# Performance work log

Measured on AMD Instinct MI355X. Metric: run time of the kernel, lower is better.

## Reference

```python
import jax, jax.numpy as jnp
import numpy as np

B, L, QD, H, D = 2, 2048, 1024, 16, 64  # batch, seq, q_dim, heads, head_dim
INNER = H * D


def rms_norm(x, scale):
    # matches torch RMSNorm: mean over last dim in fp32, eps=1e-6, learned scale
    rrms = jax.lax.rsqrt(jnp.mean(x.astype(jnp.float32) ** 2, axis=-1, keepdims=True) + 1e-6)
    return (x * rrms).astype(x.dtype) * scale


def apply_rope(xq, xk, pe):
    # pe: [1,1,L,D//2,2,2] rotation-matrix pairs (FLUX-style)
    def rot(x):
        xs = x.reshape(*x.shape[:-1], D // 2, 1, 2)  # B H L D/2 1 2
        out = pe[..., 0] * xs[..., 0] + pe[..., 1] * xs[..., 1]  # B H L D/2 2
        return out.reshape(x.shape).astype(x.dtype)
    return rot(xq), rot(xk)


def setup_inputs() -> dict:
    key = jax.random.key(0)
    ks = jax.random.split(key, 6)
    s = 0.02
    return {
        "x": jax.random.normal(ks[0], (B, L, QD), jnp.float32),
        "pe": jax.random.normal(ks[1], (1, 1, L, D // 2, 2, 2), jnp.float32),
        "Wq": jax.random.normal(ks[2], (INNER, QD), jnp.float32) * s,
        "Wkv": jax.random.normal(ks[3], (2 * INNER, QD), jnp.float32) * s,
        "Wproj": jax.random.normal(ks[4], (QD, INNER), jnp.float32) * s,
        "bproj": jnp.zeros((QD,), jnp.float32),
        "q_scale": jnp.ones((D,), jnp.float32),
        "k_scale": jnp.ones((D,), jnp.float32),
    }


def reference(x, pe, Wq, Wkv, Wproj, bproj, q_scale, k_scale):
    # q/kv projections (self-attention: context = x)
    q = jnp.einsum('blc,ec->ble', x, Wq).reshape(B, L, H, D).transpose(0, 2, 1, 3)  # B H L D
    kv = jnp.einsum('blc,ec->ble', x, Wkv).reshape(B, L, 2, H, D)  # layout (K H D)
    k = kv[:, :, 0].transpose(0, 2, 1, 3)  # B H L D
    v = kv[:, :, 1].transpose(0, 2, 1, 3)  # B H L D
    # per-head QK RMSNorm
    q = rms_norm(q, q_scale)
    k = rms_norm(k, k_scale)
    # RoPE then scaled dot-product attention
    q, k = apply_rope(q, k, pe)
    scores = jnp.einsum('bhqd,bhkd->bhqk', q, k) / np.float32(np.sqrt(D))
    attn = jax.nn.softmax(scores, axis=-1)
    o = jnp.einsum('bhqk,bhkd->bhqd', attn, v)
    o = o.transpose(0, 2, 1, 3).reshape(B, L, INNER)  # B L (H D)
    return o @ Wproj.T + bproj
```

## Files before the change

kernel.cpp:

```cpp
#include <hip/hip_runtime.h>
#include <hip/hip_bf16.h>
#include <stdint.h>

#define BB 2
#define LL 2048
#define QDIM 1024
#define NH 16
#define HD 64

using bf16x8 = __attribute__((ext_vector_type(8))) __bf16;
using bf16x2 = __attribute__((ext_vector_type(2))) __bf16;
using f32x4  = __attribute__((ext_vector_type(4))) float;
using u16x8  = __attribute__((ext_vector_type(8))) unsigned short;
using u32x2  = __attribute__((ext_vector_type(2))) uint32_t;

__device__ __forceinline__ unsigned short f2bf(float f) {
  return __builtin_bit_cast(unsigned short, (__bf16)f);
}
__device__ __forceinline__ float bf2f(unsigned short h) {
  uint32_t u = ((uint32_t)h) << 16;
  return __builtin_bit_cast(float, u);
}
__device__ __forceinline__ uint32_t pkbf2(float a, float b) {
  bf16x2 v = { (__bf16)a, (__bf16)b };
  return __builtin_bit_cast(uint32_t, v);
}

__device__ __forceinline__ void gload_lds16(const void* g, void* l) {
  __builtin_amdgcn_global_load_lds((__attribute__((address_space(1))) void*)g,
                                   (__attribute__((address_space(3))) void*)l,
                                   16, 0, 0);
}

__global__ __launch_bounds__(256) void k_cast_bf16(const float* __restrict__ in,
                                                   unsigned short* __restrict__ out, int n) {
  int i = (blockIdx.x * 256 + threadIdx.x) * 8;
  if (i >= n) return;
  float4 a = *reinterpret_cast<const float4*>(in + i);
  float4 b = *reinterpret_cast<const float4*>(in + i + 4);
  u16x8 o;
  o[0] = f2bf(a.x); o[1] = f2bf(a.y); o[2] = f2bf(a.z); o[3] = f2bf(a.w);
  o[4] = f2bf(b.x); o[5] = f2bf(b.y); o[6] = f2bf(b.z); o[7] = f2bf(b.w);
  *reinterpret_cast<u16x8*>(out + i) = o;
}

__global__ __launch_bounds__(256) void k_gemm_qkv(const unsigned short* __restrict__ A,
                                                  const unsigned short* __restrict__ Bw,
                                                  unsigned short* __restrict__ qk,
                                                  unsigned short* __restrict__ vT) {
  __shared__ unsigned short As[2][128 * 32];
  __shared__ unsigned short Bs[2][128 * 32];
  const int t = threadIdx.x;
  const int lane = t & 63, w = t >> 6;
  const int wm = w >> 1, wn = w & 1;
  const int g = lane >> 4, r16 = lane & 15;
  const size_t am0 = (size_t)blockIdx.x * 128;
  const size_t bn0 = (size_t)blockIdx.y * 128;
  const int K = 1024;

  f32x4 acc[4][4] = {};

  const int o0 = t * 16, row0 = o0 >> 6, cb0 = o0 & 63;
  const int o1 = 4096 + t * 16, row1 = o1 >> 6, cb1 = o1 & 63;

  gload_lds16(A  + (am0 + row0) * K + (cb0 >> 1), (char*)&As[0][0] + o0);
  gload_lds16(A  + (am0 + row1) * K + (cb1 >> 1), (char*)&As[0][0] + o1);
  gload_lds16(Bw + (bn0 + row0) * K + (cb0 >> 1), (char*)&Bs[0][0] + o0);
  gload_lds16(Bw + (bn0 + row1) * K + (cb1 >> 1), (char*)&Bs[0][0] + o1);
  __syncthreads();

  for (int kb = 0; kb < K; kb += 32) {
    const int cur = (kb >> 5) & 1;
    if (kb + 32 < K) {
      const int nxt = cur ^ 1;
      gload_lds16(A  + (am0 + row0) * K + kb + 32 + (cb0 >> 1), (char*)&As[nxt][0] + o0);
      gload_lds16(A  + (am0 + row1) * K + kb + 32 + (cb1 >> 1), (char*)&As[nxt][0] + o1);
      gload_lds16(Bw + (bn0 + row0) * K + kb + 32 + (cb0 >> 1), (char*)&Bs[nxt][0] + o0);
      gload_lds16(Bw + (bn0 + row1) * K + kb + 32 + (cb1 >> 1), (char*)&Bs[nxt][0] + o1);
    }
    bf16x8 af[4], bfr[4];
#pragma unroll
    for (int i = 0; i < 4; ++i)
      af[i] = *reinterpret_cast<const bf16x8*>((const char*)&As[cur][0] + (wm * 64 + i * 16 + r16) * 64 + g * 16);
#pragma unroll
    for (int j = 0; j < 4; ++j)
      bfr[j] = *reinterpret_cast<const bf16x8*>((const char*)&Bs[cur][0] + (wn * 64 + j * 16 + r16) * 64 + g * 16);
#pragma unroll
    for (int i = 0; i < 4; ++i)
#pragma unroll
      for (int j = 0; j < 4; ++j)
        acc[i][j] = __builtin_amdgcn_mfma_f32_16x16x32_bf16(af[i], bfr[j], acc[i][j], 0, 0, 0);
    __syncthreads();
  }

#pragma unroll
  for (int i = 0; i < 4; ++i)
#pragma unroll
    for (int j = 0; j < 4; ++j) {
      size_t row = am0 + wm * 64 + i * 16 + g * 4;
      int col = (int)bn0 + wn * 64 + j * 16 + r16;
      if (col < 2048) {
#pragma unroll
        for (int r = 0; r < 4; ++r) qk[(row + r) * 2048 + col] = f2bf(acc[i][j][r]);
      } else {
        int e = col - 2048, h = e >> 6, d = e & 63;
        int b = (int)(row >> 11), l2 = (int)(row & 2047);
        ushort4 pk;
        pk.x = f2bf(acc[i][j][0]); pk.y = f2bf(acc[i][j][1]);
        pk.z = f2bf(acc[i][j][2]); pk.w = f2bf(acc[i][j][3]);
        *reinterpret_cast<ushort4*>(vT + ((size_t)(b * 16 + h) * 64 + d) * 2048 + l2) = pk;
      }
    }
}

__global__ __launch_bounds__(256) void k_gemm_proj(const unsigned short* __restrict__ A,
                                                   const unsigned short* __restrict__ Bw,
                                                   float* __restrict__ Cf,
                                                   const float* __restrict__ bias) {
  __shared__ unsigned short As[2][64 * 32];
  __shared__ unsigned short Bs[2][128 * 32];
  const int t = threadIdx.x;
  const int lane = t & 63, w = t >> 6;
  const int wm = w >> 1, wn = w & 1;
  const int g = lane >> 4, r16 = lane & 15;
  const size_t am0 = (size_t)blockIdx.x * 64;
  const size_t bn0 = (size_t)blockIdx.y * 128;
  const int K = 1024;

  f32x4 acc[2][4] = {};

  const int oa = t * 16, rowa = oa >> 6, cba = oa & 63;
  const int ob0 = t * 16, rowb0 = ob0 >> 6, cbb0 = ob0 & 63;
  const int ob1 = 4096 + t * 16, rowb1 = ob1 >> 6, cbb1 = ob1 & 63;

  gload_lds16(A  + (am0 + rowa)  * K + (cba  >> 1), (char*)&As[0][0] + oa);
  gload_lds16(Bw + (bn0 + rowb0) * K + (cbb0 >> 1), (char*)&Bs[0][0] + ob0);
  gload_lds16(Bw + (bn0 + rowb1) * K + (cbb1 >> 1), (char*)&Bs[0][0] + ob1);
  __syncthreads();

  for (int kb = 0; kb < K; kb += 32) {
    const int cur = (kb >> 5) & 1;
    if (kb + 32 < K) {
      const int nxt = cur ^ 1;
      gload_lds16(A  + (am0 + rowa)  * K + kb + 32 + (cba  >> 1), (char*)&As[nxt][0] + oa);
      gload_lds16(Bw + (bn0 + rowb0) * K + kb + 32 + (cbb0 >> 1), (char*)&Bs[nxt][0] + ob0);
      gload_lds16(Bw + (bn0 + rowb1) * K + kb + 32 + (cbb1 >> 1), (char*)&Bs[nxt][0] + ob1);
    }
    bf16x8 af[2], bfr[4];
#pragma unroll
    for (int i = 0; i < 2; ++i)
      af[i] = *reinterpret_cast<const bf16x8*>((const char*)&As[cur][0] + (wm * 32 + i * 16 + r16) * 64 + g * 16);
#pragma unroll
    for (int j = 0; j < 4; ++j)
      bfr[j] = *reinterpret_cast<const bf16x8*>((const char*)&Bs[cur][0] + (wn * 64 + j * 16 + r16) * 64 + g * 16);
#pragma unroll
    for (int i = 0; i < 2; ++i)
#pragma unroll
      for (int j = 0; j < 4; ++j)
        acc[i][j] = __builtin_amdgcn_mfma_f32_16x16x32_bf16(af[i], bfr[j], acc[i][j], 0, 0, 0);
    __syncthreads();
  }

#pragma unroll
  for (int i = 0; i < 2; ++i)
#pragma unroll
    for (int j = 0; j < 4; ++j) {
      size_t row = am0 + wm * 32 + i * 16 + g * 4;
      int col = (int)bn0 + wn * 64 + j * 16 + r16;
#pragma unroll
      for (int r = 0; r < 4; ++r) Cf[(row + r) * 1024 + col] = acc[i][j][r] + bias[col];
    }
}

__global__ __launch_bounds__(256) void k_norm_rope(unsigned short* __restrict__ qkbuf,
                                                   const float* __restrict__ pe,
                                                   const float* __restrict__ qs,
                                                   const float* __restrict__ ks) {
  const float S2 = 0.125f * 1.44269504f;
  const int row = blockIdx.x;
  const int l = row & (LL - 1);
  const int t = threadIdx.x, w = t >> 6, lane = t & 63;
  const int hgrp = lane >> 5, dp = lane & 31;
  const size_t base = (size_t)row * 2048;
  const float4 pev = *reinterpret_cast<const float4*>(pe + ((size_t)l * 32 + dp) * 4);
  const float2 qsv0 = *reinterpret_cast<const float2*>(qs + dp * 2);
  const float2 ksv = *reinterpret_cast<const float2*>(ks + dp * 2);
  const float2 qsv = { qsv0.x * S2, qsv0.y * S2 };

#pragma unroll
  for (int pass = 0; pass < 4; ++pass) {
    const int isK = pass >> 1;
    const int h = w * 4 + (pass & 1) * 2 + hgrp;
    unsigned short* p = qkbuf + base + isK * 1024 + h * 64 + dp * 2;
    uint32_t v = *reinterpret_cast<uint32_t*>(p);
    float xe = bf2f((unsigned short)(v & 0xffff)), xo = bf2f((unsigned short)(v >> 16));
    float s = xe * xe + xo * xo;
#pragma unroll
    for (int mk = 1; mk < 32; mk <<= 1) s += __shfl_xor(s, mk);
    float rr = rsqrtf(s * (1.0f / 64.0f) + 1e-6f);
    float sx = isK ? ksv.x : qsv.x, sy = isK ? ksv.y : qsv.y;
    float ne = xe * rr * sx, no = xo * rr * sy;
    float oe = pev.x * ne + pev.y * no;
    float oo = pev.z * ne + pev.w * no;
    *reinterpret_cast<uint32_t*>(p) = (uint32_t)f2bf(oe) | ((uint32_t)f2bf(oo) << 16);
  }
}

__global__ __launch_bounds__(256, 2) void k_flash(const unsigned short* __restrict__ qkbuf,
                                                  const unsigned short* __restrict__ vT,
                                                  unsigned short* __restrict__ ob) {
  __shared__ unsigned short Ktile[2][64 * 64];
  __shared__ unsigned short Vtile[2][64 * 64];
  __shared__ unsigned short Plds[4][2][16 * 64];
  const int t = threadIdx.x, w = t >> 6, lane = t & 63;
  const int g = lane >> 4, r16 = lane & 15;
  const int id = blockIdx.x;
  const int bh = (id & 7) + (((id >> 3) & 3) << 3);
  const int lt = id >> 5;
  const int b = bh >> 4, h = bh & 15;
  const int l0 = lt * 128 + w * 16;
  const size_t qkb = (size_t)b * LL * 2048;
  const unsigned short* Qp = qkbuf + qkb + (size_t)(l0 + r16) * 2048 + h * 64;
  const unsigned short* Kbase = qkbuf + qkb + 1024 + h * 64;
  const unsigned short* Vbase = vT + (size_t)bh * 64 * 2048;

  bf16x8 qf[2][2];
  qf[0][0] = *reinterpret_cast<const bf16x8*>(Qp + g * 8);
  qf[0][1] = *reinterpret_cast<const bf16x8*>(Qp + 32 + g * 8);
  qf[1][0] = *reinterpret_cast<const bf16x8*>(Qp + (size_t)64 * 2048 + g * 8);
  qf[1][1] = *reinterpret_cast<const bf16x8*>(Qp + (size_t)64 * 2048 + 32 + g * 8);

  f32x4 oacc[2][4] = {};
  float m[2] = {-1e30f, -1e30f}, lsum[2] = {0.f, 0.f};

  char* Pw0 = (char*)&Plds[w][0][0];
  char* Pw1 = (char*)&Plds[w][1][0];
  const int pswz = (r16 & 7) << 4;
  const int prow = r16 * 128;
  const int wr0 = prow + ((0 * 32 + g * 8) ^ pswz);
  const int wr1 = prow + ((1 * 32 + g * 8) ^ pswz);
  const int wr2 = prow + ((2 * 32 + g * 8) ^ pswz);
  const int wr3 = prow + ((3 * 32 + g * 8) ^ pswz);
  const int rd0 = prow + ((g * 16) ^ pswz);
  const int rd1 = prow + ((64 + g * 16) ^ pswz);

  const int so0 = t * 16, sr0 = so0 >> 7, sl0 = (so0 & 127) ^ ((sr0 & 7) << 4);
  const int so1 = 4096 + t * 16, sr1 = so1 >> 7, sl1 = (so1 & 127) ^ ((sr1 & 7) << 4);

  gload_lds16(Kbase + (size_t)sr0 * 2048 + (sl0 >> 1), (char*)&Ktile[0][0] + so0);
  gload_lds16(Kbase + (size_t)sr1 * 2048 + (sl1 >> 1), (char*)&Ktile[0][0] + so1);
  gload_lds16(Vbase + (size_t)sr0 * 2048 + (sl0 >> 1), (char*)&Vtile[0][0] + so0);
  gload_lds16(Vbase + (size_t)sr1 * 2048 + (sl1 >> 1), (char*)&Vtile[0][0] + so1);
  __syncthreads();

  const int kswz = (r16 & 7) << 4;

  for (int kt = 0; kt < LL; kt += 64) {
    const int cur = (kt >> 6) & 1;
    if (kt + 64 < LL) {
      const int nxt = cur ^ 1;
      gload_lds16(Kbase + (size_t)(kt + 64 + sr0) * 2048 + (sl0 >> 1), (char*)&Ktile[nxt][0] + so0);
      gload_lds16(Kbase + (size_t)(kt + 64 + sr1) * 2048 + (sl1 >> 1), (char*)&Ktile[nxt][0] + so1);
      gload_lds16(Vbase + (size_t)sr0 * 2048 + kt + 64 + (sl0 >> 1), (char*)&Vtile[nxt][0] + so0);
      gload_lds16(Vbase + (size_t)sr1 * 2048 + kt + 64 + (sl1 >> 1), (char*)&Vtile[nxt][0] + so1);
    }
    const char* Kt = (const char*)&Ktile[cur][0];
    const char* Vt = (const char*)&Vtile[cur][0];

    f32x4 s[2][4];
#pragma unroll
    for (int kb = 0; kb < 4; ++kb) {
      const char* kp = Kt + (kb * 16 + r16) * 128;
      bf16x8 ka0 = *reinterpret_cast<const bf16x8*>(kp + ((g * 16) ^ kswz));
      bf16x8 ka1 = *reinterpret_cast<const bf16x8*>(kp + ((64 + g * 16) ^ kswz));
#pragma unroll
      for (int j = 0; j < 2; ++j) {
        f32x4 z = {};
        z = __builtin_amdgcn_mfma_f32_16x16x32_bf16(ka0, qf[j][0], z, 0, 0, 0);
        z = __builtin_amdgcn_mfma_f32_16x16x32_bf16(ka1, qf[j][1], z, 0, 0, 0);
        s[j][kb] = z;
      }
    }
#pragma unroll
    for (int j = 0; j < 2; ++j) {
      float p[16];
#pragma unroll
      for (int kb = 0; kb < 4; ++kb)
#pragma unroll
        for (int r = 0; r < 4; ++r) p[kb * 4 + r] = s[j][kb][r];
      float t0 = fmaxf(fmaxf(p[0], p[1]), p[2]);
      float t1 = fmaxf(fmaxf(p[3], p[4]), p[5]);
      float t2 = fmaxf(fmaxf(p[6], p[7]), p[8]);
      float t3 = fmaxf(fmaxf(p[9], p[10]), p[11]);
      float t4 = fmaxf(fmaxf(p[12], p[13]), p[14]);
      float tm = fmaxf(fmaxf(fmaxf(t0, t1), t2), fmaxf(fmaxf(t3, t4), p[15]));
      tm = fmaxf(tm, __shfl_xor(tm, 16));
      tm = fmaxf(tm, __shfl_xor(tm, 32));
      if (!__all(tm <= m[j] + 11.0f)) {
        float nm = fmaxf(m[j], tm);
        float alpha = __builtin_exp2f(m[j] - nm);
        lsum[j] *= alpha;
#pragma unroll
        for (int dt = 0; dt < 4; ++dt) oacc[j][dt] *= alpha;
        m[j] = nm;
      }
#pragma unroll
      for (int i = 0; i < 16; ++i) p[i] = __builtin_exp2f(p[i] - m[j]);
      float a0 = (p[0] + p[1]) + (p[2] + p[3]);
      float a1 = (p[4] + p[5]) + (p[6] + p[7]);
      float a2 = (p[8] + p[9]) + (p[10] + p[11]);
      float a3 = (p[12] + p[13]) + (p[14] + p[15]);
      float ts = (a0 + a1) + (a2 + a3);
      ts += __shfl_xor(ts, 16);
      ts += __shfl_xor(ts, 32);
      lsum[j] += ts;
      char* Pw = j ? Pw1 : Pw0;
      u32x2 wv;
      wv[0] = pkbf2(p[0],  p[1]);  wv[1] = pkbf2(p[2],  p[3]);
      *reinterpret_cast<u32x2*>(Pw + wr0) = wv;
      wv[0] = pkbf2(p[4],  p[5]);  wv[1] = pkbf2(p[6],  p[7]);
      *reinterpret_cast<u32x2*>(Pw + wr1) = wv;
      wv[0] = pkbf2(p[8],  p[9]);  wv[1] = pkbf2(p[10], p[11]);
      *reinterpret_cast<u32x2*>(Pw + wr2) = wv;
      wv[0] = pkbf2(p[12], p[13]); wv[1] = pkbf2(p[14], p[15]);
      *reinterpret_cast<u32x2*>(Pw + wr3) = wv;
    }
    __asm__ __volatile__("s_waitcnt lgkmcnt(0)" ::: "memory");
    bf16x8 pb[2][2];
    pb[0][0] = *reinterpret_cast<const bf16x8*>(Pw0 + rd0);
    pb[0][1] = *reinterpret_cast<const bf16x8*>(Pw0 + rd1);
    pb[1][0] = *reinterpret_cast<const bf16x8*>(Pw1 + rd0);
    pb[1][1] = *reinterpret_cast<const bf16x8*>(Pw1 + rd1);
#pragma unroll
    for (int dt = 0; dt < 4; ++dt) {
      const char* vp = Vt + (dt * 16 + r16) * 128;
      bf16x8 va0 = *reinterpret_cast<const bf16x8*>(vp + ((g * 16) ^ kswz));
      bf16x8 va1 = *reinterpret_cast<const bf16x8*>(vp + ((64 + g * 16) ^ kswz));
#pragma unroll
      for (int j = 0; j < 2; ++j) {
        oacc[j][dt] = __builtin_amdgcn_mfma_f32_16x16x32_bf16(va0, pb[j][0], oacc[j][dt], 0, 0, 0);
        oacc[j][dt] = __builtin_amdgcn_mfma_f32_16x16x32_bf16(va1, pb[j][1], oacc[j][dt], 0, 0, 0);
      }
    }
    __syncthreads();
  }

#pragma unroll
  for (int j = 0; j < 2; ++j) {
    const float inv = 1.0f / lsum[j];
    const size_t orow = (size_t)(b * LL + l0 + j * 64 + r16) * 1024 + h * 64;
#pragma unroll
    for (int dt = 0; dt < 4; ++dt) {
      ushort4 pk;
      pk.x = f2bf(oacc[j][dt][0] * inv); pk.y = f2bf(oacc[j][dt][1] * inv);
      pk.z = f2bf(oacc[j][dt][2] * inv); pk.w = f2bf(oacc[j][dt][3] * inv);
      *reinterpret_cast<ushort4*>(ob + orow + dt * 16 + g * 4) = pk;
    }
  }
}

extern "C" void kernel_launch(void* const* d_in, const int* in_sizes, int n_in,
                              void* d_out, int out_size, void* d_ws, size_t ws_size,
                              hipStream_t stream) {
  const float* x     = (const float*)d_in[0];
  const float* pe    = (const float*)d_in[1];
  const float* Wq    = (const float*)d_in[2];
  const float* Wkv   = (const float*)d_in[3];
  const float* Wproj = (const float*)d_in[4];
  const float* bproj = (const float*)d_in[5];
  const float* qs    = (const float*)d_in[6];
  const float* ks    = (const float*)d_in[7];
  float* out = (float*)d_out;

  char* ws = (char*)d_ws;
  unsigned short* xb     = (unsigned short*)(ws);
  unsigned short* Wall   = (unsigned short*)(ws + 8u  * 1024 * 1024);
  unsigned short* Wprojb = (unsigned short*)(ws + 14u * 1024 * 1024);
  unsigned short* qk     = (unsigned short*)(ws + 16u * 1024 * 1024);
  unsigned short* vT     = (unsigned short*)(ws + 32u * 1024 * 1024);
  unsigned short* ob     = (unsigned short*)(ws + 40u * 1024 * 1024);

  k_cast_bf16<<<4194304 / 2048, 256, 0, stream>>>(x, xb, 4194304);
  k_cast_bf16<<<1048576 / 2048, 256, 0, stream>>>(Wq, Wall, 1048576);
  k_cast_bf16<<<2097152 / 2048, 256, 0, stream>>>(Wkv, Wall + 1048576, 2097152);
  k_cast_bf16<<<1048576 / 2048, 256, 0, stream>>>(Wproj, Wprojb, 1048576);

  k_gemm_qkv<<<dim3(32, 24), 256, 0, stream>>>(xb, Wall, qk, vT);

  k_norm_rope<<<BB * LL, 256, 0, stream>>>(qk, pe, qs, ks);
  k_flash<<<512, 256, 0, stream>>>(qk, vT, ob);

  k_gemm_proj<<<dim3(64, 8), 256, 0, stream>>>(ob, Wprojb, out, bproj);
}
```

Measured before the change: 236.5 us.

## Fuse QK RMSNorm and RoPE into QKV GEMM epilogue, merge casts

Four cast launches become one kernel that picks its source buffer by block index. The separate norm+RoPE kernel is removed. Its work now runs in the QKV GEMM epilogue, using lane shuffles for the per-head sum of squares and for the RoPE pair swap. The V transpose is staged through swizzled LDS so vT gets 16-byte coalesced stores. This saves a full read-modify-write pass over the Q/K buffer and several launches, at the cost of a heavier epilogue with scattered pe loads and 2-byte qk stores.

```diff
diff --git a/kernel.cpp b/kernel.cpp
--- a/kernel.cpp
+++ b/kernel.cpp
@@ -32,59 +32,75 @@
                                    16, 0, 0);
 }
 
-__global__ __launch_bounds__(256) void k_cast_bf16(const float* __restrict__ in,
-                                                   unsigned short* __restrict__ out, int n) {
-  int i = (blockIdx.x * 256 + threadIdx.x) * 8;
-  if (i >= n) return;
-  float4 a = *reinterpret_cast<const float4*>(in + i);
-  float4 b = *reinterpret_cast<const float4*>(in + i + 4);
+__global__ __launch_bounds__(256) void k_cast_all(const float* __restrict__ x,
+                                                  const float* __restrict__ wq,
+                                                  const float* __restrict__ wkv,
+                                                  const float* __restrict__ wp,
+                                                  unsigned short* __restrict__ xb,
+                                                  unsigned short* __restrict__ wall,
+                                                  unsigned short* __restrict__ wpb) {
+  const int blk = blockIdx.x;
+  const float* src; unsigned short* dst; int base;
+  if (blk < 2048)      { src = x;   dst = xb;             base = blk; }
+  else if (blk < 2560) { src = wq;  dst = wall;           base = blk - 2048; }
+  else if (blk < 3584) { src = wkv; dst = wall + 1048576; base = blk - 2560; }
+  else                 { src = wp;  dst = wpb;            base = blk - 3584; }
+  const int i = base * 2048 + threadIdx.x * 8;
+  float4 a = *reinterpret_cast<const float4*>(src + i);
+  float4 b = *reinterpret_cast<const float4*>(src + i + 4);
   u16x8 o;
   o[0] = f2bf(a.x); o[1] = f2bf(a.y); o[2] = f2bf(a.z); o[3] = f2bf(a.w);
   o[4] = f2bf(b.x); o[5] = f2bf(b.y); o[6] = f2bf(b.z); o[7] = f2bf(b.w);
-  *reinterpret_cast<u16x8*>(out + i) = o;
+  *reinterpret_cast<u16x8*>(dst + i) = o;
 }
 
 __global__ __launch_bounds__(256) void k_gemm_qkv(const unsigned short* __restrict__ A,
                                                   const unsigned short* __restrict__ Bw,
                                                   unsigned short* __restrict__ qk,
-                                                  unsigned short* __restrict__ vT) {
-  __shared__ unsigned short As[2][128 * 32];
-  __shared__ unsigned short Bs[2][128 * 32];
+                                                  unsigned short* __restrict__ vT,
+                                                  const float* __restrict__ pe,
+                                                  const float* __restrict__ qs,
+                                                  const float* __restrict__ ks) {
+  __shared__ char smem[32768];
   const int t = threadIdx.x;
   const int lane = t & 63, w = t >> 6;
   const int wm = w >> 1, wn = w & 1;
   const int g = lane >> 4, r16 = lane & 15;
   const size_t am0 = (size_t)blockIdx.x * 128;
-  const size_t bn0 = (size_t)blockIdx.y * 128;
+  const int bn0 = blockIdx.y * 128;
   const int K = 1024;
+  const float S2 = 0.125f * 1.44269504f;
 
   f32x4 acc[4][4] = {};
 
   const int o0 = t * 16, row0 = o0 >> 6, cb0 = o0 & 63;
   const int o1 = 4096 + t * 16, row1 = o1 >> 6, cb1 = o1 & 63;
 
-  gload_lds16(A  + (am0 + row0) * K + (cb0 >> 1), (char*)&As[0][0] + o0);
-  gload_lds16(A  + (am0 + row1) * K + (cb1 >> 1), (char*)&As[0][0] + o1);
-  gload_lds16(Bw + (bn0 + row0) * K + (cb0 >> 1), (char*)&Bs[0][0] + o0);
-  gload_lds16(Bw + (bn0 + row1) * K + (cb1 >> 1), (char*)&Bs[0][0] + o1);
+  char* As0 = smem;
+  char* Bs0 = smem + 16384;
+
+  gload_lds16(A  + (am0 + row0) * K + (cb0 >> 1), As0 + o0);
+  gload_lds16(A  + (am0 + row1) * K + (cb1 >> 1), As0 + o1);
+  gload_lds16(Bw + ((size_t)bn0 + row0) * K + (cb0 >> 1), Bs0 + o0);
+  gload_lds16(Bw + ((size_t)bn0 + row1) * K + (cb1 >> 1), Bs0 + o1);
   __syncthreads();
 
   for (int kb = 0; kb < K; kb += 32) {
     const int cur = (kb >> 5) & 1;
     if (kb + 32 < K) {
       const int nxt = cur ^ 1;
-      gload_lds16(A  + (am0 + row0) * K + kb + 32 + (cb0 >> 1), (char*)&As[nxt][0] + o0);
-      gload_lds16(A  + (am0 + row1) * K + kb + 32 + (cb1 >> 1), (char*)&As[nxt][0] + o1);
-      gload_lds16(Bw + (bn0 + row0) * K + kb + 32 + (cb0 >> 1), (char*)&Bs[nxt][0] + o0);
-      gload_lds16(Bw + (bn0 + row1) * K + kb + 32 + (cb1 >> 1), (char*)&Bs[nxt][0] + o1);
+      gload_lds16(A  + (am0 + row0) * K + kb + 32 + (cb0 >> 1), As0 + nxt * 8192 + o0);
+      gload_lds16(A  + (am0 + row1) * K + kb + 32 + (cb1 >> 1), As0 + nxt * 8192 + o1);
+      gload_lds16(Bw + ((size_t)bn0 + row0) * K + kb + 32 + (cb0 >> 1), Bs0 + nxt * 8192 + o0);
+      gload_lds16(Bw + ((size_t)bn0 + row1) * K + kb + 32 + (cb1 >> 1), Bs0 + nxt * 8192 + o1);
     }
     bf16x8 af[4], bfr[4];
 #pragma unroll
     for (int i = 0; i < 4; ++i)
-      af[i] = *reinterpret_cast<const bf16x8*>((const char*)&As[cur][0] + (wm * 64 + i * 16 + r16) * 64 + g * 16);
+      af[i] = *reinterpret_cast<const bf16x8*>(As0 + cur * 8192 + (wm * 64 + i * 16 + r16) * 64 + g * 16);
 #pragma unroll
     for (int j = 0; j < 4; ++j)
-      bfr[j] = *reinterpret_cast<const bf16x8*>((const char*)&Bs[cur][0] + (wn * 64 + j * 16 + r16) * 64 + g * 16);
+      bfr[j] = *reinterpret_cast<const bf16x8*>(Bs0 + cur * 8192 + (wn * 64 + j * 16 + r16) * 64 + g * 16);
 #pragma unroll
     for (int i = 0; i < 4; ++i)
 #pragma unroll
@@ -93,24 +109,70 @@
     __syncthreads();
   }
 
-#pragma unroll
-  for (int i = 0; i < 4; ++i)
+  if (bn0 < 2048) {
+    const bool isQ = (bn0 < 1024);
+    float sc[4];
 #pragma unroll
     for (int j = 0; j < 4; ++j) {
-      size_t row = am0 + wm * 64 + i * 16 + g * 4;
-      int col = (int)bn0 + wn * 64 + j * 16 + r16;
-      if (col < 2048) {
-#pragma unroll
-        for (int r = 0; r < 4; ++r) qk[(row + r) * 2048 + col] = f2bf(acc[i][j][r]);
-      } else {
-        int e = col - 2048, h = e >> 6, d = e & 63;
-        int b = (int)(row >> 11), l2 = (int)(row & 2047);
-        ushort4 pk;
-        pk.x = f2bf(acc[i][j][0]); pk.y = f2bf(acc[i][j][1]);
-        pk.z = f2bf(acc[i][j][2]); pk.w = f2bf(acc[i][j][3]);
-        *reinterpret_cast<ushort4*>(vT + ((size_t)(b * 16 + h) * 64 + d) * 2048 + l2) = pk;
-      }
-    }
+      const int d = j * 16 + r16;
+      sc[j] = isQ ? qs[d] * S2 : ks[d];
+    }
+#pragma unroll
+    for (int i = 0; i < 4; ++i) {
+      const size_t rowb = am0 + wm * 64 + i * 16 + g * 4;
+      float rr[4];
+#pragma unroll
+      for (int r = 0; r < 4; ++r) {
+        float s = 0.f;
+#pragma unroll
+        for (int j = 0; j < 4; ++j) s += acc[i][j][r] * acc[i][j][r];
+        s += __shfl_xor(s, 1); s += __shfl_xor(s, 2);
+        s += __shfl_xor(s, 4); s += __shfl_xor(s, 8);
+        rr[r] = rsqrtf(s * (1.0f / 64.0f) + 1e-6f);
+      }
+#pragma unroll
+      for (int j = 0; j < 4; ++j) {
+        const int d = j * 16 + r16;
+        const int dp = d >> 1, odd = d & 1;
+        const int col = bn0 + wn * 64 + d;
+#pragma unroll
+        for (int r = 0; r < 4; ++r) {
+          const int l = (int)((rowb + r) & (LL - 1));
+          float v = acc[i][j][r] * rr[r] * sc[j];
+          float pr = __shfl_xor(v, 1);
+          float xe = odd ? pr : v, xo = odd ? v : pr;
+          const float2 pe2 = *reinterpret_cast<const float2*>(pe + ((size_t)l * 32 + dp) * 4 + odd * 2);
+          qk[(rowb + r) * 2048 + col] = f2bf(pe2.x * xe + pe2.y * xo);
+        }
+      }
+    }
+  } else {
+    unsigned short* Tr = (unsigned short*)smem;
+#pragma unroll
+    for (int i = 0; i < 4; ++i)
+#pragma unroll
+      for (int j = 0; j < 4; ++j) {
+        const int c = wn * 64 + j * 16 + r16;
+        const int rw = wm * 64 + i * 16 + g * 4;
+        const int byte = c * 256 + ((rw * 2) ^ ((c & 7) << 4));
+        u32x2 pk;
+        pk[0] = pkbf2(acc[i][j][0], acc[i][j][1]);
+        pk[1] = pkbf2(acc[i][j][2], acc[i][j][3]);
+        *reinterpret_cast<u32x2*>((char*)Tr + byte) = pk;
+      }
+    __syncthreads();
+    const int b = (int)(am0 >> 11);
+    const int lbase = (int)(am0 & (LL - 1));
+#pragma unroll
+    for (int p = 0; p < 8; ++p) {
+      const int c = p * 16 + (t >> 4);
+      const int ch = t & 15;
+      const int byte = c * 256 + ((ch * 16) ^ ((c & 7) << 4));
+      u16x8 val = *reinterpret_cast<const u16x8*>((char*)Tr + byte);
+      const int e = bn0 + c - 2048, h = e >> 6, d = e & 63;
+      *reinterpret_cast<u16x8*>(vT + ((size_t)(b * 16 + h) * 64 + d) * 2048 + lbase + ch * 8) = val;
+    }
+  }
 }
 
 __global__ __launch_bounds__(256) void k_gemm_proj(const unsigned short* __restrict__ A,
@@ -170,40 +232,6 @@
 #pragma unroll
       for (int r = 0; r < 4; ++r) Cf[(row + r) * 1024 + col] = acc[i][j][r] + bias[col];
     }
-}
-
-__global__ __launch_bounds__(256) void k_norm_rope(unsigned short* __restrict__ qkbuf,
-                                                   const float* __restrict__ pe,
-                                                   const float* __restrict__ qs,
-                                                   const float* __restrict__ ks) {
-  const float S2 = 0.125f * 1.44269504f;
-  const int row = blockIdx.x;
-  const int l = row & (LL - 1);
-  const int t = threadIdx.x, w = t >> 6, lane = t & 63;
-  const int hgrp = lane >> 5, dp = lane & 31;
-  const size_t base = (size_t)row * 2048;
-  const float4 pev = *reinterpret_cast<const float4*>(pe + ((size_t)l * 32 + dp) * 4);
-  const float2 qsv0 = *reinterpret_cast<const float2*>(qs + dp * 2);
-  const float2 ksv = *reinterpret_cast<const float2*>(ks + dp * 2);
-  const float2 qsv = { qsv0.x * S2, qsv0.y * S2 };
-
-#pragma unroll
-  for (int pass = 0; pass < 4; ++pass) {
-    const int isK = pass >> 1;
-    const int h = w * 4 + (pass & 1) * 2 + hgrp;
-    unsigned short* p = qkbuf + base + isK * 1024 + h * 64 + dp * 2;
-    uint32_t v = *reinterpret_cast<uint32_t*>(p);
-    float xe = bf2f((unsigned short)(v & 0xffff)), xo = bf2f((unsigned short)(v >> 16));
-    float s = xe * xe + xo * xo;
-#pragma unroll
-    for (int mk = 1; mk < 32; mk <<= 1) s += __shfl_xor(s, mk);
-    float rr = rsqrtf(s * (1.0f / 64.0f) + 1e-6f);
-    float sx = isK ? ksv.x : qsv.x, sy = isK ? ksv.y : qsv.y;
-    float ne = xe * rr * sx, no = xo * rr * sy;
-    float oe = pev.x * ne + pev.y * no;
-    float oo = pev.z * ne + pev.w * no;
-    *reinterpret_cast<uint32_t*>(p) = (uint32_t)f2bf(oe) | ((uint32_t)f2bf(oo) << 16);
-  }
 }
 
 __global__ __launch_bounds__(256, 2) void k_flash(const unsigned short* __restrict__ qkbuf,
@@ -380,15 +408,8 @@
   unsigned short* vT     = (unsigned short*)(ws + 32u * 1024 * 1024);
   unsigned short* ob     = (unsigned short*)(ws + 40u * 1024 * 1024);
 
-  k_cast_bf16<<<4194304 / 2048, 256, 0, stream>>>(x, xb, 4194304);
-  k_cast_bf16<<<1048576 / 2048, 256, 0, stream>>>(Wq, Wall, 1048576);
-  k_cast_bf16<<<2097152 / 2048, 256, 0, stream>>>(Wkv, Wall + 1048576, 2097152);
-  k_cast_bf16<<<1048576 / 2048, 256, 0, stream>>>(Wproj, Wprojb, 1048576);
-
-  k_gemm_qkv<<<dim3(32, 24), 256, 0, stream>>>(xb, Wall, qk, vT);
-
-  k_norm_rope<<<BB * LL, 256, 0, stream>>>(qk, pe, qs, ks);
+  k_cast_all<<<4096, 256, 0, stream>>>(x, Wq, Wkv, Wproj, xb, Wall, Wprojb);
+  k_gemm_qkv<<<dim3(32, 24), 256, 0, stream>>>(xb, Wall, qk, vT, pe, qs, ks);
   k_flash<<<512, 256, 0, stream>>>(qk, vT, ob);
-
   k_gemm_proj<<<dim3(64, 8), 256, 0, stream>>>(ob, Wprojb, out, bproj);
 }
```

Result: faster. 223.6 us (-5.5%).
